# Optimization experiments

Hardware: AMD Instinct MI355X
Metric: run time of the kernel (lower is better)

Reference implementation:

```python
import jax, jax.numpy as jnp
import numpy as np

WS = 7   # window_size
SS = 3   # shift_size = window_size // 2
NH = 16  # num_heads


def _rel_pos_index(ws):
    coords = np.stack(np.meshgrid(np.arange(ws), np.arange(ws), indexing='ij'))  # (2, ws, ws)
    cf = coords.reshape(2, -1)
    rel = (cf[:, :, None] - cf[:, None, :]).transpose(1, 2, 0)
    rel[:, :, 0] += ws - 1
    rel[:, :, 1] += ws - 1
    rel[:, :, 0] *= 2 * ws - 1
    return rel.sum(-1)  # (ws*ws, ws*ws) int

REL_IDX = _rel_pos_index(WS)


def _attn_mask(h, w, ws, ss):
    img = np.zeros((h, w))
    sls = (slice(0, -ws), slice(-ws, -ss), slice(-ss, None))
    cnt = 0
    for i in sls:
        for j in sls:
            img[i, j] = cnt
            cnt += 1
    mw = img.reshape(h // ws, ws, w // ws, ws).transpose(0, 2, 1, 3).reshape(-1, ws * ws)
    d = mw[:, None, :] - mw[:, :, None]  # (nW, N, N)
    return np.where(d != 0, -100.0, 0.0).astype(np.float32)


def _part(x, ws):
    b, h, w, c = x.shape
    return x.reshape(b, h // ws, ws, w // ws, ws, c).transpose(0, 1, 3, 2, 4, 5).reshape(-1, ws * ws, c)


def _rev(win, ws, h, w):
    c = win.shape[-1]
    b = win.shape[0] // ((h // ws) * (w // ws))
    return win.reshape(b, h // ws, w // ws, ws, ws, c).transpose(0, 1, 3, 2, 4, 5).reshape(b, h, w, c)


def _ln(x, g, b):
    m = x.mean(-1, keepdims=True)
    v = x.var(-1, keepdims=True)
    return (x - m) / jnp.sqrt(v + 1e-5) * g + b


def _wattn(x, qkv_w, qkv_b, proj_w, proj_b, table, mask):
    B_, N, C = x.shape
    hd = C // NH
    scale = hd ** -0.5
    qkv = (x @ qkv_w.T + qkv_b).reshape(B_, N, 3, NH, hd).transpose(2, 0, 3, 1, 4)
    q, k, v = qkv[0] * scale, qkv[1], qkv[2]  # (B_, NH, N, hd)
    attn = jnp.einsum('bhnd,bhmd->bhnm', q, k)
    bias = table[REL_IDX.reshape(-1)].reshape(N, N, NH).transpose(2, 0, 1)  # (NH, N, N)
    attn = attn + bias[None]
    if mask is not None:
        nW = mask.shape[0]
        attn = (attn.reshape(B_ // nW, nW, NH, N, N) + mask[None, :, None]).reshape(B_, NH, N, N)
    attn = jax.nn.softmax(attn, axis=-1)
    out = jnp.einsum('bhnm,bhmd->bhnd', attn, v).transpose(0, 2, 1, 3).reshape(B_, N, C)
    return out @ proj_w.T + proj_b


def _mlp(x, w1, b1, w2, b2):
    return jax.nn.gelu(x @ w1.T + b1, approximate=False) @ w2.T + b2


def _forward(x, w_norm1_g, w_norm1_b, w_qkv_w, w_qkv_b, w_proj_w, w_proj_b, w_table,
             w_norm2_g, w_norm2_b, w_fc1_w, w_fc1_b, w_fc2_w, w_fc2_b,
             sw_norm1_g, sw_norm1_b, sw_qkv_w, sw_qkv_b, sw_proj_w, sw_proj_b, sw_table,
             sw_norm2_g, sw_norm2_b, sw_fc1_w, sw_fc1_b, sw_fc2_w, sw_fc2_b):
    b, c, h, w = x.shape
    x = jnp.transpose(x, (0, 2, 3, 1)).reshape(b, h * w, c)  # (B, HW, C)
    shortcut = x
    xn = _ln(x, w_norm1_g, w_norm1_b).reshape(b, h, w, c)
    aw = _wattn(_part(xn, WS), w_qkv_w, w_qkv_b, w_proj_w, w_proj_b, w_table, None)
    x = shortcut + _rev(aw, WS, h, w).reshape(b, h * w, c)
    x = x + _mlp(_ln(x, w_norm2_g, w_norm2_b), w_fc1_w, w_fc1_b, w_fc2_w, w_fc2_b)
    # shifted-window branch (shift_size > 0 since min(h,w) > window_size)
    xn = _ln(x, sw_norm1_g, sw_norm1_b)
    mask = jnp.asarray(_attn_mask(h, w, WS, SS))
    shifted = jnp.roll(xn.reshape(b, h, w, c), (-SS, -SS), axis=(1, 2))
    sa = _wattn(_part(shifted, WS), sw_qkv_w, sw_qkv_b, sw_proj_w, sw_proj_b, sw_table, mask)
    shifted = jnp.roll(_rev(sa, WS, h, w), (SS, SS), axis=(1, 2)).reshape(b, h * w, c)
    # NOTE: source adds the residual to the *normalized* activations here; kept faithful.
    x = xn + shifted
    x = x + _mlp(_ln(x, sw_norm2_g, sw_norm2_b), sw_fc1_w, sw_fc1_b, sw_fc2_w, sw_fc2_b)
    return x.reshape(b, h, w, c)


def setup_inputs() -> dict:
    key = jax.random.key(0)
    ks = jax.random.split(key, 32)
    B, C, H, W = 8, 512, 56, 56
    Cm = 4 * C
    T = (2 * WS - 1) ** 2

    def rn(k, shape, s=0.02):
        return jax.random.normal(k, shape, jnp.float32) * s

    d = {'x': jax.random.normal(ks[0], (B, C, H, W), jnp.float32)}
    for i, p in enumerate(['w', 'sw']):
        o = 1 + i * 6
        d[p + '_norm1_g'] = jnp.ones((C,), jnp.float32)
        d[p + '_norm1_b'] = jnp.zeros((C,), jnp.float32)
        d[p + '_qkv_w'] = rn(ks[o], (3 * C, C))
        d[p + '_qkv_b'] = jnp.zeros((3 * C,), jnp.float32)
        d[p + '_proj_w'] = rn(ks[o + 1], (C, C))
        d[p + '_proj_b'] = jnp.zeros((C,), jnp.float32)
        d[p + '_table'] = rn(ks[o + 2], (T, NH))
        d[p + '_norm2_g'] = jnp.ones((C,), jnp.float32)
        d[p + '_norm2_b'] = jnp.zeros((C,), jnp.float32)
        d[p + '_fc1_w'] = rn(ks[o + 3], (Cm, C))
        d[p + '_fc1_b'] = jnp.zeros((Cm,), jnp.float32)
        d[p + '_fc2_w'] = rn(ks[o + 4], (C, Cm))
        d[p + '_fc2_b'] = jnp.zeros((C,), jnp.float32)
    return d


def reference(x, w_norm1_g, w_norm1_b, w_qkv_w, w_qkv_b, w_proj_w, w_proj_b, w_table,
              w_norm2_g, w_norm2_b, w_fc1_w, w_fc1_b, w_fc2_w, w_fc2_b,
              sw_norm1_g, sw_norm1_b, sw_qkv_w, sw_qkv_b, sw_proj_w, sw_proj_b, sw_table,
              sw_norm2_g, sw_norm2_b, sw_fc1_w, sw_fc1_b, sw_fc2_w, sw_fc2_b):
    return _forward(x, w_norm1_g, w_norm1_b, w_qkv_w, w_qkv_b, w_proj_w, w_proj_b, w_table,
                    w_norm2_g, w_norm2_b, w_fc1_w, w_fc1_b, w_fc2_w, w_fc2_b,
                    sw_norm1_g, sw_norm1_b, sw_qkv_w, sw_qkv_b, sw_proj_w, sw_proj_b, sw_table,
                    sw_norm2_g, sw_norm2_b, sw_fc1_w, sw_fc1_b, sw_fc2_w, sw_fc2_b)
```

## Files before the change

### kernel.cpp

```cpp
#include <hip/hip_runtime.h>
#include <hip/hip_bf16.h>

using bf16 = __hip_bfloat16;

#define B_      8
#define C_      512
#define H_      56
#define W_      56
#define HW_     3136
#define M_      25088
#define NH_     16
#define HD_     32
#define WS_     7
#define NT_     49

typedef __attribute__((ext_vector_type(8))) short bf16x8;
typedef __attribute__((ext_vector_type(4))) float f32x4;

#define AS1(p) ((const __attribute__((address_space(1))) void*)(p))
#define AS3(p) ((__attribute__((address_space(3))) void*)(p))

__device__ inline float bf2f(const bf16 v) {
    unsigned short u = *reinterpret_cast<const unsigned short*>(&v);
    return __uint_as_float((unsigned)u << 16);
}
__device__ inline unsigned short f2bfu(float f) {
    bf16 h = __float2bfloat16(f);
    return *reinterpret_cast<unsigned short*>(&h);
}
__device__ inline float rdv(const float* p) { return *p; }
__device__ inline float rdv(const bf16* p)  { return bf2f(*p); }
__device__ inline void stv(float* p, float v) { *p = v; }
__device__ inline void stv(bf16* p, float v)  { *p = __float2bfloat16(v); }

__device__ inline float gelu_t(float v) {
    const float u = v * (0.79788456080286536f + 0.035677408136300125f * v * v);
    const float e = __expf(2.0f * u);
    return 0.5f * v * (2.0f - 2.0f / (e + 1.0f));
}

__global__ void k_detect(const void* g1, int* flag) {
    const unsigned short* u = (const unsigned short*)g1;
    *flag = (u[0] == 0x3F80u) ? 1 : 0;
}

struct WArgs {
    const void* src[26];
    bf16*       dst[26];
    int         n[26];
};
__global__ __launch_bounds__(256) void k_convert_all(WArgs a, const int* flag) {
    const int isb = *flag;
    const int gid = blockIdx.x * 256 + threadIdx.x;
    const int stride = gridDim.x * 256;
    #pragma unroll 1
    for (int w = 0; w < 26; ++w) {
        const int n = a.n[w];
        bf16* d = a.dst[w];
        if (isb) {
            const unsigned short* s = (const unsigned short*)a.src[w];
            for (int i = gid; i < n; i += stride) ((unsigned short*)d)[i] = s[i];
        } else {
            const float* s = (const float*)a.src[w];
            for (int i = gid; i < n; i += stride) d[i] = __float2bfloat16(s[i]);
        }
    }
}

__global__ __launch_bounds__(256) void k_transpose_in(const void* xin, bf16* X,
                                                      const int* flag) {
    __shared__ float tile[32][33];
    const int isb = *flag;
    const int p0 = blockIdx.x * 32, c0 = blockIdx.y * 32, b = blockIdx.z;
    const int tp = threadIdx.x & 31, tc = threadIdx.x >> 5;
    const size_t ibase = (size_t)b * C_ * HW_;
    #pragma unroll
    for (int i = 0; i < 4; ++i) {
        const int c = tc + i * 8;
        const size_t idx = ibase + (size_t)(c0 + c) * HW_ + p0 + tp;
        tile[c][tp] = isb ? bf2f(((const bf16*)xin)[idx]) : ((const float*)xin)[idx];
    }
    __syncthreads();
    const int wc = threadIdx.x & 31, wp = threadIdx.x >> 5;
    bf16* dst = X + (size_t)b * HW_ * C_;
    #pragma unroll
    for (int i = 0; i < 4; ++i) {
        const int p = wp + i * 8;
        dst[(size_t)(p0 + p) * C_ + c0 + wc] = __float2bfloat16(tile[wc][p]);
    }
}

typedef __attribute__((ext_vector_type(8))) unsigned short u16x8;
__global__ __launch_bounds__(512) void k_layernorm(const bf16* __restrict__ X,
                                                   const bf16* __restrict__ g,
                                                   const bf16* __restrict__ bta,
                                                   bf16* __restrict__ XN) {
    const int wid  = threadIdx.x >> 6;
    const int lane = threadIdx.x & 63;
    const size_t tok = (size_t)blockIdx.x * 8 + wid;
    const size_t base = tok * C_ + lane * 8;

    const u16x8 u = *reinterpret_cast<const u16x8*>(X + base);
    float v[8];
    float s = 0.f, s2 = 0.f;
    #pragma unroll
    for (int e = 0; e < 8; ++e) {
        v[e] = __uint_as_float((unsigned)u[e] << 16);
        s += v[e]; s2 += v[e] * v[e];
    }
    #pragma unroll
    for (int d = 1; d <= 32; d <<= 1) { s += __shfl_xor(s, d); s2 += __shfl_xor(s2, d); }
    const float m  = s * (1.0f / C_);
    const float va = s2 * (1.0f / C_) - m * m;
    const float r  = rsqrtf(va + 1e-5f);

    const u16x8 ug = *reinterpret_cast<const u16x8*>(g   + lane * 8);
    const u16x8 ub = *reinterpret_cast<const u16x8*>(bta + lane * 8);
    u16x8 o;
    #pragma unroll
    for (int e = 0; e < 8; ++e) {
        const float gf = __uint_as_float((unsigned)ug[e] << 16);
        const float bf = __uint_as_float((unsigned)ub[e] << 16);
        o[e] = f2bfu((v[e] - m) * r * gf + bf);
    }
    *reinterpret_cast<u16x8*>(XN + base) = o;
}

template <typename TADD, typename TO, bool GELU, bool ADD, bool FINAL>
__global__ __launch_bounds__(512, 2) void k_gemm8(const bf16* __restrict__ A,
                                                  const bf16* __restrict__ Wt,
                                                  const bf16* __restrict__ bias,
                                                  const TADD* __restrict__ addp,
                                                  TO* __restrict__ out,
                                                  const int* flag,
                                                  int N, int K) {
    __shared__ bf16 sA[2][2][128 * 64];
    __shared__ bf16 sB[2][2][128 * 64];
    const int tid  = threadIdx.x;
    const int lane = tid & 63;
    const int wid  = tid >> 6;
    const int wr   = wid >> 2;
    const int wc2  = wid & 3;
    const int bh   = wc2 >> 1;
    const int brl  = (wc2 & 1) * 64;

    const int nwg  = gridDim.x;
    const int orig = blockIdx.x;
    const int nx = nwg >> 3, rr_ = nwg & 7;
    const int xcd = orig & 7, offw = orig >> 3;
    const int wg = (xcd < rr_ ? xcd * (nx + 1) : rr_ * (nx + 1) + (xcd - rr_) * nx) + offw;
    const int gx = N >> 8;
    const int m0 = (wg / gx) * 256, n0 = (wg % gx) * 256;

    const f32x4 vz = {0.f, 0.f, 0.f, 0.f};
    f32x4 acc[8][4];
    #pragma unroll
    for (int i = 0; i < 8; ++i)
        #pragma unroll
        for (int j = 0; j < 4; ++j) acc[i][j] = vz;

    const int sr8  = lane >> 3;
    const int schk = (lane & 7) ^ sr8;
    const bf16* gA0 = A  + (size_t)(m0 + sr8) * K + schk * 8;
    const bf16* gB0 = Wt + (size_t)(n0 + sr8) * K + schk * 8;

    const int l15 = lane & 15, g4 = lane >> 4;
    const int NTL = K >> 6;
    const int NITER = NTL >> 1;

    auto stageA = [&](int d, int h, int T) {
        const int kt = T << 6;
        #pragma unroll
        for (int p = 0; p < 2; ++p) {
            const int q = wid * 2 + p;
            __builtin_amdgcn_global_load_lds(
                AS1(gA0 + (size_t)(h * 128 + q * 8) * K + kt),
                AS3(&sA[d][h][q * 512]), 16, 0, 0);
        }
    };
    auto stageB = [&](int d, int h, int T) {
        const int kt = T << 6;
        #pragma unroll
        for (int p = 0; p < 2; ++p) {
            const int q = wid * 2 + p;
            __builtin_amdgcn_global_load_lds(
                AS1(gB0 + (size_t)(h * 128 + q * 8) * K + kt),
                AS3(&sB[d][h][q * 512]), 16, 0, 0);
        }
    };

    stageA(0, 0, 0); stageA(0, 1, 0);
    stageB(0, 0, 0); stageB(0, 1, 0);
    stageB(1, 0, 1); stageB(1, 1, 1);
    asm volatile("s_waitcnt vmcnt(4)" ::: "memory");
    __builtin_amdgcn_s_barrier();

    #pragma unroll 1
    for (int it = 0; it < NITER; ++it) {
        const bool nl = (it < NITER - 1);
        #pragma unroll
        for (int half = 0; half < 2; ++half) {
            bf16x8 bfr[4][2];
            #pragma unroll
            for (int q = 0; q < 4; ++q) {
                if (q == 0) {
                    #pragma unroll
                    for (int ks = 0; ks < 2; ++ks) {
                        const int ch = ((ks << 2) | g4) ^ (l15 & 7);
                        #pragma unroll
                        for (int j = 0; j < 4; ++j) {
                            const int r = brl + j * 16 + l15;
                            bfr[j][ks] = *reinterpret_cast<const bf16x8*>(&sB[half][bh][r * 64 + ch * 8]);
                        }
                    }
                }
                bf16x8 af[2][2];
                #pragma unroll
                for (int ks = 0; ks < 2; ++ks) {
                    const int ch = ((ks << 2) | g4) ^ (l15 & 7);
                    #pragma unroll
                    for (int ii = 0; ii < 2; ++ii) {
                        const int r = (q * 2 + ii) * 16 + l15;
                        af[ii][ks] = *reinterpret_cast<const bf16x8*>(&sA[half][wr][r * 64 + ch * 8]);
                    }
                }
                if (half == 0) {
                    if (q == 0)            { stageA(1, 0, 2 * it + 1); stageA(1, 1, 2 * it + 1); }
                    else if (q == 1 && nl) { stageB(0, 0, 2 * it + 2); }
                    else if (q == 2 && nl) { stageB(0, 1, 2 * it + 2); }
                } else {
                    if (q == 0 && nl)      { stageA(0, 0, 2 * it + 2); }
                    else if (q == 1 && nl) { stageA(0, 1, 2 * it + 2); }
                    else if (q == 2 && nl) { stageB(1, 0, 2 * it + 3); }
                    else if (q == 3 && nl) { stageB(1, 1, 2 * it + 3); }
                }
                __builtin_amdgcn_s_barrier();
                asm volatile("s_waitcnt lgkmcnt(0)" ::: "memory");
                __builtin_amdgcn_s_setprio(1);
                #pragma unroll
                for (int ks = 0; ks < 2; ++ks)
                    #pragma unroll
                    for (int ii = 0; ii < 2; ++ii)
                        #pragma unroll
                        for (int j = 0; j < 4; ++j)
                            acc[q * 2 + ii][j] = __builtin_amdgcn_mfma_f32_16x16x32_bf16(
                                af[ii][ks], bfr[j][ks], acc[q * 2 + ii][j], 0, 0, 0);
                __builtin_amdgcn_s_setprio(0);
                if (q == 3) {
                    if (half == 0) {
                        if (nl) asm volatile("s_waitcnt vmcnt(4)" ::: "memory");
                        else    asm volatile("s_waitcnt vmcnt(0)" ::: "memory");
                    } else if (nl) {
                        asm volatile("s_waitcnt vmcnt(4)" ::: "memory");
                    }
                }
                __builtin_amdgcn_s_barrier();
            }
        }
    }

    int obf = 0;
    if constexpr (FINAL) obf = *flag;
    const int colBase = n0 + wc2 * 64 + l15;
    const int rowTop  = m0 + wr * 128 + g4 * 4;
    float bc[4];
    #pragma unroll
    for (int j = 0; j < 4; ++j) bc[j] = bf2f(bias[colBase + j * 16]);
    #pragma unroll
    for (int i = 0; i < 8; ++i) {
        #pragma unroll
        for (int r = 0; r < 4; ++r) {
            const int row = rowTop + i * 16 + r;
            #pragma unroll
            for (int j = 0; j < 4; ++j) {
                const int col = colBase + j * 16;
                float v = acc[i][j][r] + bc[j];
                if constexpr (GELU) v = gelu_t(v);
                if constexpr (ADD)  v += rdv(&addp[(size_t)row * N + col]);
                if constexpr (FINAL) {
                    if (obf) ((bf16*)(void*)out)[(size_t)row * N + col] = __float2bfloat16(v);
                    else     ((float*)(void*)out)[(size_t)row * N + col] = v;
                } else {
                    stv(&out[(size_t)row * N + col], v);
                }
            }
        }
    }
}

template <typename TADD, typename TO, bool GELU, bool ADD, bool FINAL>
__global__ __launch_bounds__(512, 2) void k_gemm_mfma(const bf16* __restrict__ A,
                                                      const bf16* __restrict__ Wt,
                                                      const bf16* __restrict__ bias,
                                                      const TADD* __restrict__ addp,
                                                      TO* __restrict__ out,
                                                      const int* flag,
                                                      int N, int K) {
    __shared__ bf16 sA[3][256 * 64];
    __shared__ bf16 sB[3][128 * 64];
    const int tid  = threadIdx.x;
    const int lane = tid & 63;
    const int wid  = tid >> 6;
    const int wr   = wid >> 1;
    const int wc2  = wid & 1;

    const int nwg  = gridDim.x;
    const int orig = blockIdx.x;
    const int nx = nwg >> 3, rr_ = nwg & 7;
    const int xcd = orig & 7, offw = orig >> 3;
    const int wg = (xcd < rr_ ? xcd * (nx + 1) : rr_ * (nx + 1) + (xcd - rr_) * nx) + offw;
    const int gx = N >> 7;
    const int m0 = (wg / gx) * 256, n0 = (wg % gx) * 128;

    const f32x4 vz = {0.f, 0.f, 0.f, 0.f};
    f32x4 acc[4][4];
    #pragma unroll
    for (int i = 0; i < 4; ++i)
        #pragma unroll
        for (int j = 0; j < 4; ++j) acc[i][j] = vz;

    const int sr8  = lane >> 3;
    const int schk = (lane & 7) ^ sr8;
    const bf16* gA0 = A  + (size_t)(m0 + sr8) * K + schk * 8;
    const bf16* gB0 = Wt + (size_t)(n0 + sr8) * K + schk * 8;

    const int l15 = lane & 15, g4 = lane >> 4;
    const int NTLE = K >> 6;

    #pragma unroll
    for (int tt = 0; tt < 3; ++tt) {
        const int kt = tt << 6;
        #pragma unroll
        for (int p = 0; p < 4; ++p) {
            const int q = wid * 4 + p;
            __builtin_amdgcn_global_load_lds(AS1(gA0 + (size_t)(q * 8) * K + kt),
                                             AS3(&sA[tt][q * 512]), 16, 0, 0);
        }
        #pragma unroll
        for (int p = 0; p < 2; ++p) {
            const int q = wid * 2 + p;
            __builtin_amdgcn_global_load_lds(AS1(gB0 + (size_t)(q * 8) * K + kt),
                                             AS3(&sB[tt][q * 512]), 16, 0, 0);
        }
    }

    for (int t = 0; t < NTLE; ++t) {
        const int rem = NTLE - 1 - t;
        if (rem >= 2)      asm volatile("s_waitcnt vmcnt(12)" ::: "memory");
        else if (rem == 1) asm volatile("s_waitcnt vmcnt(6)"  ::: "memory");
        else               asm volatile("s_waitcnt vmcnt(0)"  ::: "memory");
        __builtin_amdgcn_s_barrier();

        const int buf = t % 3;
        bf16x8 bfr[4][2];
        #pragma unroll
        for (int ks = 0; ks < 2; ++ks) {
            const int ch = ((ks << 2) | g4) ^ (l15 & 7);
            #pragma unroll
            for (int j = 0; j < 4; ++j) {
                const int rowB = wc2 * 64 + j * 16 + l15;
                bfr[j][ks] = *reinterpret_cast<const bf16x8*>(&sB[buf][rowB * 64 + ch * 8]);
            }
        }
        const int ch0 = g4 ^ (l15 & 7);
        const int ch1 = (4 | g4) ^ (l15 & 7);
        __builtin_amdgcn_s_setprio(1);
        #pragma unroll
        for (int i = 0; i < 4; ++i) {
            const int rowA = wr * 64 + i * 16 + l15;
            const bf16x8 a0 = *reinterpret_cast<const bf16x8*>(&sA[buf][rowA * 64 + ch0 * 8]);
            const bf16x8 a1 = *reinterpret_cast<const bf16x8*>(&sA[buf][rowA * 64 + ch1 * 8]);
            #pragma unroll
            for (int j = 0; j < 4; ++j) {
                acc[i][j] = __builtin_amdgcn_mfma_f32_16x16x32_bf16(a0, bfr[j][0], acc[i][j], 0, 0, 0);
                acc[i][j] = __builtin_amdgcn_mfma_f32_16x16x32_bf16(a1, bfr[j][1], acc[i][j], 0, 0, 0);
            }
        }
        __builtin_amdgcn_s_setprio(0);

        asm volatile("s_waitcnt lgkmcnt(0)" ::: "memory");
        __builtin_amdgcn_s_barrier();

        const int tn = t + 3;
        if (tn < NTLE) {
            const int kt = tn << 6;
            #pragma unroll
            for (int p = 0; p < 4; ++p) {
                const int q = wid * 4 + p;
                __builtin_amdgcn_global_load_lds(AS1(gA0 + (size_t)(q * 8) * K + kt),
                                                 AS3(&sA[buf][q * 512]), 16, 0, 0);
            }
            #pragma unroll
            for (int p = 0; p < 2; ++p) {
                const int q = wid * 2 + p;
                __builtin_amdgcn_global_load_lds(AS1(gB0 + (size_t)(q * 8) * K + kt),
                                                 AS3(&sB[buf][q * 512]), 16, 0, 0);
            }
        }
    }

    int obf = 0;
    if constexpr (FINAL) obf = *flag;
    const int colBase = n0 + wc2 * 64 + l15;
    const int rowTop  = m0 + wr * 64 + g4 * 4;
    float bc[4];
    #pragma unroll
    for (int j = 0; j < 4; ++j) bc[j] = bf2f(bias[colBase + j * 16]);
    #pragma unroll
    for (int i = 0; i < 4; ++i) {
        #pragma unroll
        for (int r = 0; r < 4; ++r) {
            const int row = rowTop + i * 16 + r;
            #pragma unroll
            for (int j = 0; j < 4; ++j) {
                const int col = colBase + j * 16;
                float v = acc[i][j][r] + bc[j];
                if constexpr (GELU) v = gelu_t(v);
                if constexpr (ADD)  v += rdv(&addp[(size_t)row * N + col]);
                if constexpr (FINAL) {
                    if (obf) ((bf16*)(void*)out)[(size_t)row * N + col] = __float2bfloat16(v);
                    else     ((float*)(void*)out)[(size_t)row * N + col] = v;
                } else {
                    stv(&out[(size_t)row * N + col], v);
                }
            }
        }
    }
}

__global__ __launch_bounds__(256) void k_mktbl(const bf16* __restrict__ table,
                                               bf16* __restrict__ out, int shifted) {
    const int bh = blockIdx.x;
    const int cls = bh >> 4, h = bh & 15;
    const int rowE = shifted ? (cls >> 1) : 0;
    const int colE = shifted ? (cls & 1) : 0;
    for (int e = threadIdx.x; e < 64 * 64; e += 256) {
        const int i = e >> 6, j = e & 63;
        float v;
        if (i < NT_ && j < NT_) {
            const int yi = i / WS_, xi = i % WS_, yj = j / WS_, xj = j % WS_;
            const int ridx = (yi - yj + 6) * 13 + (xi - xj + 6);
            v = bf2f(table[ridx * NH_ + h]);
            const int ri = (rowE ? (yi < 4 ? 1 : 2) : 0) * 3 + (colE ? (xi < 4 ? 1 : 2) : 0);
            const int rj = (rowE ? (yj < 4 ? 1 : 2) : 0) * 3 + (colE ? (xj < 4 ? 1 : 2) : 0);
            if (ri != rj) v -= 100.f;
        } else if (j >= NT_) {
            v = -3e30f;
        } else {
            v = 0.f;
        }
        out[((size_t)bh << 12) + e] = __float2bfloat16(v);
    }
}

template <int SS, bool SHIFTED>
__global__ __launch_bounds__(64) void k_attn_mfma(const bf16* __restrict__ QKV,
                                                  const bf16* __restrict__ tbl,
                                                  bf16* __restrict__ O) {
    __shared__ __align__(16) short uQK[5120];
    __shared__ __align__(16) short uVt[2304];
    __shared__ int toks[NT_];
    short* Qs = uQK;
    short* Ks = uQK + 2560;
    short* Ps = uQK;

    const int lane = threadIdx.x;
    const int head = blockIdx.x & 15;
    const int win  = blockIdx.x >> 4;
    const int bl = win >> 6, w64 = win & 63;
    const int wy = w64 >> 3, wx = w64 & 7;

    if (lane < NT_) {
        const int dy = lane / WS_, dx = lane % WS_;
        const int sr = wy * WS_ + dy, scn = wx * WS_ + dx;
        const int r = (sr + SS) % H_, c = (scn + SS) % W_;
        toks[lane] = bl * HW_ + r * W_ + c;
    }
    __syncthreads();

    const int g4 = lane >> 4, l15 = lane & 15;
    const int tsg = lane >> 2, csg = (lane & 3) * 8;

    #pragma unroll
    for (int rr = 0; rr < 4; ++rr) {
        const int t = rr * 16 + tsg;
        bf16x8 qv = {0,0,0,0,0,0,0,0}, kv = {0,0,0,0,0,0,0,0}, vv = {0,0,0,0,0,0,0,0};
        if (t < NT_) {
            const bf16* base = QKV + (size_t)toks[t] * 1536 + head * HD_ + csg;
            qv = *reinterpret_cast<const bf16x8*>(base);
            kv = *reinterpret_cast<const bf16x8*>(base + 512);
            vv = *reinterpret_cast<const bf16x8*>(base + 1024);
        }
        *reinterpret_cast<bf16x8*>(&Qs[t * 40 + csg]) = qv;
        *reinterpret_cast<bf16x8*>(&Ks[t * 40 + csg]) = kv;
        #pragma unroll
        for (int e = 0; e < 8; ++e) uVt[(csg + e) * 72 + t] = ((const short*)&vv)[e];
    }
    __syncthreads();

    bf16x8 aq[4], bk[4];
    #pragma unroll
    for (int f = 0; f < 4; ++f) {
        aq[f] = *reinterpret_cast<const bf16x8*>(&Qs[(f * 16 + l15) * 40 + g4 * 8]);
        bk[f] = *reinterpret_cast<const bf16x8*>(&Ks[(f * 16 + l15) * 40 + g4 * 8]);
    }
    const f32x4 vz = {0.f, 0.f, 0.f, 0.f};
    f32x4 sacc[4][4];
    #pragma unroll
    for (int qi = 0; qi < 4; ++qi)
        #pragma unroll
        for (int kj = 0; kj < 4; ++kj)
            sacc[qi][kj] = __builtin_amdgcn_mfma_f32_16x16x32_bf16(aq[qi], bk[kj], vz, 0, 0, 0);
    __syncthreads();

    const int cls = SHIFTED ? (((wy == 7) ? 2 : 0) + ((wx == 7) ? 1 : 0)) : 0;
    const bf16* tb = tbl + (((size_t)(cls * NH_ + head)) << 12);
    const float scale = 0.17677669529663687f;
    #pragma unroll
    for (int qi = 0; qi < 4; ++qi) {
        #pragma unroll
        for (int r = 0; r < 4; ++r) {
            const int i = qi * 16 + g4 * 4 + r;
            const bf16* trow = tb + (i << 6);
            float sv[4];
            #pragma unroll
            for (int kj = 0; kj < 4; ++kj)
                sv[kj] = sacc[qi][kj][r] * scale + bf2f(trow[kj * 16 + l15]);
            float mx = fmaxf(fmaxf(sv[0], sv[1]), fmaxf(sv[2], sv[3]));
            #pragma unroll
            for (int d = 1; d <= 8; d <<= 1) mx = fmaxf(mx, __shfl_xor(mx, d));
            float p[4], sum = 0.f;
            #pragma unroll
            for (int kj = 0; kj < 4; ++kj) { p[kj] = __expf(sv[kj] - mx); sum += p[kj]; }
            #pragma unroll
            for (int d = 1; d <= 8; d <<= 1) sum += __shfl_xor(sum, d);
            const float inv = 1.0f / sum;
            #pragma unroll
            for (int kj = 0; kj < 4; ++kj)
                Ps[i * 72 + kj * 16 + l15] = (short)f2bfu(p[kj] * inv);
        }
    }
    __syncthreads();

    f32x4 oacc[4][2];
    #pragma unroll
    for (int qi = 0; qi < 4; ++qi) { oacc[qi][0] = vz; oacc[qi][1] = vz; }
    #pragma unroll
    for (int ks = 0; ks < 2; ++ks) {
        bf16x8 bv[2];
        #pragma unroll
        for (int dj = 0; dj < 2; ++dj)
            bv[dj] = *reinterpret_cast<const bf16x8*>(&uVt[(dj * 16 + l15) * 72 + ks * 32 + g4 * 8]);
        #pragma unroll
        for (int qi = 0; qi < 4; ++qi) {
            const bf16x8 ap = *reinterpret_cast<const bf16x8*>(&Ps[(qi * 16 + l15) * 72 + ks * 32 + g4 * 8]);
            #pragma unroll
            for (int dj = 0; dj < 2; ++dj)
                oacc[qi][dj] = __builtin_amdgcn_mfma_f32_16x16x32_bf16(ap, bv[dj], oacc[qi][dj], 0, 0, 0);
        }
    }
    #pragma unroll
    for (int qi = 0; qi < 4; ++qi) {
        #pragma unroll
        for (int r = 0; r < 4; ++r) {
            const int i = qi * 16 + g4 * 4 + r;
            if (i < NT_) {
                const size_t ob = (size_t)toks[i] * C_ + head * HD_ + l15;
                O[ob]      = __float2bfloat16(oacc[qi][0][r]);
                O[ob + 16] = __float2bfloat16(oacc[qi][1][r]);
            }
        }
    }
}

extern "C" void kernel_launch(void* const* d_in, const int* in_sizes, int n_in,
                              void* d_out, int out_size, void* d_ws, size_t ws_size,
                              hipStream_t stream) {
    (void)out_size; (void)ws_size;
    char* ws = (char*)d_ws;
    const size_t WEIGHT_RESERVE = 12651520;
    bf16*  WC   = (bf16*)ws;
    int*   FLG  = (int*)(ws + WEIGHT_RESERVE);
    bf16*  TBL1 = (bf16*)(ws + WEIGHT_RESERVE + 1024);
    bf16*  TBL2 = (bf16*)(ws + WEIGHT_RESERVE + 1024 + 131072);
    bf16*  X    = (bf16*)(ws + WEIGHT_RESERVE + 656384);
    bf16*  XN   = X + (size_t)M_ * C_;
    char*  BIG  = (char*)(XN + (size_t)M_ * C_);

    size_t offs[27];
    size_t off = 0;
    for (int i = 1; i < n_in && i < 27; ++i) { offs[i] = off; off += (size_t)((in_sizes[i] + 7) & ~7); }
    auto wc = [&](int i) { return (const bf16*)(WC + offs[i]); };

    k_detect<<<1, 1, 0, stream>>>(d_in[1], FLG);
    {
        WArgs a;
        for (int i = 1; i < 27; ++i) {
            a.src[i - 1] = d_in[i];
            a.dst[i - 1] = WC + offs[i];
            a.n[i - 1]   = in_sizes[i];
        }
        k_convert_all<<<512, 256, 0, stream>>>(a, FLG);
    }
    k_mktbl<<<16, 256, 0, stream>>>(wc(7),  TBL1, 0);
    k_mktbl<<<64, 256, 0, stream>>>(wc(20), TBL2, 1);

    const dim3 gT(HW_ / 32, C_ / 32, B_);
    k_transpose_in<<<gT, 256, 0, stream>>>(d_in[0], X, FLG);

    bf16* QKV = (bf16*)BIG;
    bf16* ATT = (bf16*)(BIG + (size_t)M_ * 1536 * 2);
    bf16* HID = (bf16*)BIG;

    const int gQ = (1536 / 256) * (M_ / 256);
    const int gF = (2048 / 256) * (M_ / 256);
    const int gP = (512 / 128)  * (M_ / 256);
    const int gO = (512 / 256)  * (M_ / 256);
    const int gL = M_ / 8;
    const dim3 gA(B_ * 64 * NH_);

    k_layernorm<<<gL, 512, 0, stream>>>(X, wc(1), wc(2), XN);
    k_gemm8<bf16, bf16, false, false, false><<<gQ, 512, 0, stream>>>(
        XN, wc(3), wc(4), (const bf16*)nullptr, QKV, nullptr, 1536, C_);
    k_attn_mfma<0, false><<<gA, 64, 0, stream>>>(QKV, TBL1, ATT);
    k_gemm_mfma<bf16, bf16, false, true, false><<<gP, 512, 0, stream>>>(
        ATT, wc(5), wc(6), X, X, nullptr, C_, C_);
    k_layernorm<<<gL, 512, 0, stream>>>(X, wc(8), wc(9), XN);
    k_gemm8<bf16, bf16, true, false, false><<<gF, 512, 0, stream>>>(
        XN, wc(10), wc(11), (const bf16*)nullptr, HID, nullptr, 2048, C_);
    k_gemm8<bf16, bf16, false, true, false><<<gO, 512, 0, stream>>>(
        HID, wc(12), wc(13), X, X, nullptr, C_, 2048);
    k_layernorm<<<gL, 512, 0, stream>>>(X, wc(14), wc(15), XN);
    k_gemm8<bf16, bf16, false, false, false><<<gQ, 512, 0, stream>>>(
        XN, wc(16), wc(17), (const bf16*)nullptr, QKV, nullptr, 1536, C_);
    k_attn_mfma<3, true><<<gA, 64, 0, stream>>>(QKV, TBL2, ATT);
    k_gemm_mfma<bf16, bf16, false, true, false><<<gP, 512, 0, stream>>>(
        ATT, wc(18), wc(19), XN, X, nullptr, C_, C_);
    k_layernorm<<<gL, 512, 0, stream>>>(X, wc(21), wc(22), XN);
    k_gemm8<bf16, bf16, true, false, false><<<gF, 512, 0, stream>>>(
        XN, wc(23), wc(24), (const bf16*)nullptr, HID, nullptr, 2048, C_);
    k_gemm8<bf16, float, false, true, true><<<gO, 512, 0, stream>>>(
        HID, wc(25), wc(26), X, (float*)d_out, FLG, C_, 2048);
}
```

Baseline: 781.8 us.

## Replace LDS-pipelined projection GEMM with direct global-to-register MFMA kernel

The attention output projection GEMM (K=512, N=512) now uses a new kernel where each wave loads its A and B fragments straight from global memory into registers and issues MFMAs. The triple-buffered LDS staging with barriers is removed, and tiles change to 64x256 per 256-thread block. This removes LDS traffic and synchronisation overhead for a small-K GEMM. In exchange, A is re-read from global by each of the 4 waves and global loads are less coalesced, so the kernel relies more on cache bandwidth.

```diff
diff --git a/kernel.cpp b/kernel.cpp
--- a/kernel.cpp
+++ b/kernel.cpp
@@ -288,29 +288,18 @@
     }
 }
 
-template <typename TADD, typename TO, bool GELU, bool ADD, bool FINAL>
-__global__ __launch_bounds__(512, 2) void k_gemm_mfma(const bf16* __restrict__ A,
-                                                      const bf16* __restrict__ Wt,
-                                                      const bf16* __restrict__ bias,
-                                                      const TADD* __restrict__ addp,
-                                                      TO* __restrict__ out,
-                                                      const int* flag,
-                                                      int N, int K) {
-    __shared__ bf16 sA[3][256 * 64];
-    __shared__ bf16 sB[3][128 * 64];
-    const int tid  = threadIdx.x;
-    const int lane = tid & 63;
-    const int wid  = tid >> 6;
-    const int wr   = wid >> 1;
-    const int wc2  = wid & 1;
-
-    const int nwg  = gridDim.x;
-    const int orig = blockIdx.x;
-    const int nx = nwg >> 3, rr_ = nwg & 7;
-    const int xcd = orig & 7, offw = orig >> 3;
-    const int wg = (xcd < rr_ ? xcd * (nx + 1) : rr_ * (nx + 1) + (xcd - rr_) * nx) + offw;
-    const int gx = N >> 7;
-    const int m0 = (wg / gx) * 256, n0 = (wg % gx) * 128;
+template <typename TADD, bool ADD>
+__global__ __launch_bounds__(256) void k_gemm_dir(const bf16* __restrict__ A,
+                                                  const bf16* __restrict__ Wt,
+                                                  const bf16* __restrict__ bias,
+                                                  const TADD* __restrict__ addp,
+                                                  bf16* __restrict__ out,
+                                                  int N, int K) {
+    const int lane = threadIdx.x & 63;
+    const int w    = threadIdx.x >> 6;
+    const int l15  = lane & 15, g4 = lane >> 4;
+    const int m0   = (blockIdx.x >> 1) * 64;
+    const int n0   = (blockIdx.x & 1) * 256 + w * 64;
 
     const f32x4 vz = {0.f, 0.f, 0.f, 0.f};
     f32x4 acc[4][4];
@@ -319,90 +308,31 @@
         #pragma unroll
         for (int j = 0; j < 4; ++j) acc[i][j] = vz;
 
-    const int sr8  = lane >> 3;
-    const int schk = (lane & 7) ^ sr8;
-    const bf16* gA0 = A  + (size_t)(m0 + sr8) * K + schk * 8;
-    const bf16* gB0 = Wt + (size_t)(n0 + sr8) * K + schk * 8;
-
-    const int l15 = lane & 15, g4 = lane >> 4;
-    const int NTLE = K >> 6;
-
-    #pragma unroll
-    for (int tt = 0; tt < 3; ++tt) {
-        const int kt = tt << 6;
-        #pragma unroll
-        for (int p = 0; p < 4; ++p) {
-            const int q = wid * 4 + p;
-            __builtin_amdgcn_global_load_lds(AS1(gA0 + (size_t)(q * 8) * K + kt),
-                                             AS3(&sA[tt][q * 512]), 16, 0, 0);
-        }
-        #pragma unroll
-        for (int p = 0; p < 2; ++p) {
-            const int q = wid * 2 + p;
-            __builtin_amdgcn_global_load_lds(AS1(gB0 + (size_t)(q * 8) * K + kt),
-                                             AS3(&sB[tt][q * 512]), 16, 0, 0);
-        }
-    }
-
-    for (int t = 0; t < NTLE; ++t) {
-        const int rem = NTLE - 1 - t;
-        if (rem >= 2)      asm volatile("s_waitcnt vmcnt(12)" ::: "memory");
-        else if (rem == 1) asm volatile("s_waitcnt vmcnt(6)"  ::: "memory");
-        else               asm volatile("s_waitcnt vmcnt(0)"  ::: "memory");
-        __builtin_amdgcn_s_barrier();
-
-        const int buf = t % 3;
-        bf16x8 bfr[4][2];
-        #pragma unroll
-        for (int ks = 0; ks < 2; ++ks) {
-            const int ch = ((ks << 2) | g4) ^ (l15 & 7);
-            #pragma unroll
-            for (int j = 0; j < 4; ++j) {
-                const int rowB = wc2 * 64 + j * 16 + l15;
-                bfr[j][ks] = *reinterpret_cast<const bf16x8*>(&sB[buf][rowB * 64 + ch * 8]);
-            }
-        }
-        const int ch0 = g4 ^ (l15 & 7);
-        const int ch1 = (4 | g4) ^ (l15 & 7);
-        __builtin_amdgcn_s_setprio(1);
-        #pragma unroll
-        for (int i = 0; i < 4; ++i) {
-            const int rowA = wr * 64 + i * 16 + l15;
-            const bf16x8 a0 = *reinterpret_cast<const bf16x8*>(&sA[buf][rowA * 64 + ch0 * 8]);
-            const bf16x8 a1 = *reinterpret_cast<const bf16x8*>(&sA[buf][rowA * 64 + ch1 * 8]);
-            #pragma unroll
-            for (int j = 0; j < 4; ++j) {
-                acc[i][j] = __builtin_amdgcn_mfma_f32_16x16x32_bf16(a0, bfr[j][0], acc[i][j], 0, 0, 0);
-                acc[i][j] = __builtin_amdgcn_mfma_f32_16x16x32_bf16(a1, bfr[j][1], acc[i][j], 0, 0, 0);
-            }
-        }
-        __builtin_amdgcn_s_setprio(0);
-
-        asm volatile("s_waitcnt lgkmcnt(0)" ::: "memory");
-        __builtin_amdgcn_s_barrier();
-
-        const int tn = t + 3;
-        if (tn < NTLE) {
-            const int kt = tn << 6;
-            #pragma unroll
-            for (int p = 0; p < 4; ++p) {
-                const int q = wid * 4 + p;
-                __builtin_amdgcn_global_load_lds(AS1(gA0 + (size_t)(q * 8) * K + kt),
-                                                 AS3(&sA[buf][q * 512]), 16, 0, 0);
-            }
-            #pragma unroll
-            for (int p = 0; p < 2; ++p) {
-                const int q = wid * 2 + p;
-                __builtin_amdgcn_global_load_lds(AS1(gB0 + (size_t)(q * 8) * K + kt),
-                                                 AS3(&sB[buf][q * 512]), 16, 0, 0);
-            }
-        }
-    }
-
-    int obf = 0;
-    if constexpr (FINAL) obf = *flag;
-    const int colBase = n0 + wc2 * 64 + l15;
-    const int rowTop  = m0 + wr * 64 + g4 * 4;
+    const bf16* Ar[4];
+    const bf16* Br[4];
+    #pragma unroll
+    for (int f = 0; f < 4; ++f) {
+        Ar[f] = A  + (size_t)(m0 + f * 16 + l15) * K + g4 * 8;
+        Br[f] = Wt + (size_t)(n0 + f * 16 + l15) * K + g4 * 8;
+    }
+
+    #pragma unroll 4
+    for (int kt = 0; kt < K; kt += 32) {
+        bf16x8 af[4], bf_[4];
+        #pragma unroll
+        for (int f = 0; f < 4; ++f) {
+            af[f]  = *reinterpret_cast<const bf16x8*>(Ar[f] + kt);
+            bf_[f] = *reinterpret_cast<const bf16x8*>(Br[f] + kt);
+        }
+        #pragma unroll
+        for (int i = 0; i < 4; ++i)
+            #pragma unroll
+            for (int j = 0; j < 4; ++j)
+                acc[i][j] = __builtin_amdgcn_mfma_f32_16x16x32_bf16(af[i], bf_[j], acc[i][j], 0, 0, 0);
+    }
+
+    const int colBase = n0 + l15;
+    const int rowTop  = m0 + g4 * 4;
     float bc[4];
     #pragma unroll
     for (int j = 0; j < 4; ++j) bc[j] = bf2f(bias[colBase + j * 16]);
@@ -415,14 +345,8 @@
             for (int j = 0; j < 4; ++j) {
                 const int col = colBase + j * 16;
                 float v = acc[i][j][r] + bc[j];
-                if constexpr (GELU) v = gelu_t(v);
-                if constexpr (ADD)  v += rdv(&addp[(size_t)row * N + col]);
-                if constexpr (FINAL) {
-                    if (obf) ((bf16*)(void*)out)[(size_t)row * N + col] = __float2bfloat16(v);
-                    else     ((float*)(void*)out)[(size_t)row * N + col] = v;
-                } else {
-                    stv(&out[(size_t)row * N + col], v);
-                }
+                if constexpr (ADD) v += rdv(&addp[(size_t)row * N + col]);
+                out[(size_t)row * N + col] = __float2bfloat16(v);
             }
         }
     }
@@ -614,7 +538,7 @@
 
     const int gQ = (1536 / 256) * (M_ / 256);
     const int gF = (2048 / 256) * (M_ / 256);
-    const int gP = (512 / 128)  * (M_ / 256);
+    const int gD = (M_ / 64) * 2;
     const int gO = (512 / 256)  * (M_ / 256);
     const int gL = M_ / 8;
     const dim3 gA(B_ * 64 * NH_);
@@ -623,8 +547,8 @@
     k_gemm8<bf16, bf16, false, false, false><<<gQ, 512, 0, stream>>>(
         XN, wc(3), wc(4), (const bf16*)nullptr, QKV, nullptr, 1536, C_);
     k_attn_mfma<0, false><<<gA, 64, 0, stream>>>(QKV, TBL1, ATT);
-    k_gemm_mfma<bf16, bf16, false, true, false><<<gP, 512, 0, stream>>>(
-        ATT, wc(5), wc(6), X, X, nullptr, C_, C_);
+    k_gemm_dir<bf16, true><<<gD, 256, 0, stream>>>(
+        ATT, wc(5), wc(6), X, X, C_, C_);
     k_layernorm<<<gL, 512, 0, stream>>>(X, wc(8), wc(9), XN);
     k_gemm8<bf16, bf16, true, false, false><<<gF, 512, 0, stream>>>(
         XN, wc(10), wc(11), (const bf16*)nullptr, HID, nullptr, 2048, C_);
@@ -634,8 +558,8 @@
     k_gemm8<bf16, bf16, false, false, false><<<gQ, 512, 0, stream>>>(
         XN, wc(16), wc(17), (const bf16*)nullptr, QKV, nullptr, 1536, C_);
     k_attn_mfma<3, true><<<gA, 64, 0, stream>>>(QKV, TBL2, ATT);
-    k_gemm_mfma<bf16, bf16, false, true, false><<<gP, 512, 0, stream>>>(
-        ATT, wc(18), wc(19), XN, X, nullptr, C_, C_);
+    k_gemm_dir<bf16, true><<<gD, 256, 0, stream>>>(
+        ATT, wc(18), wc(19), XN, X, C_, C_);
     k_layernorm<<<gL, 512, 0, stream>>>(X, wc(21), wc(22), XN);
     k_gemm8<bf16, bf16, true, false, false><<<gF, 512, 0, stream>>>(
         XN, wc(23), wc(24), (const bf16*)nullptr, HID, nullptr, 2048, C_);
```

After: 848.2 us. +8.5%, slower.
